# Kernel optimization log

Measured on AMD Instinct MI355X. Metric: run time of the kernel, lower is better.

## Reference

```python
import jax, jax.numpy as jnp
import numpy as np

EPS = 1e-6

def wave_repr(x, global_mode):
    # x: [B,S,D]
    x = jnp.clip(x, -10.0, 10.0)
    xsq = x * x
    if global_mode:
        Gsq = jnp.sum(xsq, axis=(1, 2), keepdims=True) + EPS  # [B,1,1]
    else:
        Gsq = jnp.sum(xsq, axis=1, keepdims=True) + EPS       # [B,1,D]
    G = jnp.maximum(jnp.sqrt(Gsq), EPS)
    # NOTE: source uses torch.div(..., rounding_mode='floor') -> floor division
    ratio = jnp.clip(jnp.floor(x / G), -0.99, 0.99)
    sqrt_term = jnp.sqrt(jnp.maximum(1.0 - ratio * ratio, EPS))
    alpha = jnp.arctan2(sqrt_term, ratio)
    return G * jnp.cos(alpha), G * jnp.sin(alpha)

def gelu(x):
    return jax.nn.gelu(x, approximate=False)

def rmsnorm(x, w):
    return x * jax.lax.rsqrt(jnp.mean(x * x, axis=-1, keepdims=True) + EPS) * w

def setup_inputs() -> dict:
    key = jax.random.key(0)
    B, S, D = 4, 4096, 1024
    ks = jax.random.split(key, 16)
    s = 0.02
    p = {
        'x': jax.random.normal(ks[0], (B, S, D), jnp.float32),
        'Wa': jax.random.normal(ks[1], (D, D)) * s, 'ba': jnp.zeros((D,)),
        'Wp': jax.random.normal(ks[2], (D, D)) * s, 'bp': jnp.zeros((D,)),
        'gate_bias': jnp.zeros((D,)),
        'w1r': jax.random.normal(ks[3], (D, 4 * D)) * s, 'b1r': jnp.zeros((4 * D,)),
        'w2r': jax.random.normal(ks[4], (4 * D, D)) * s, 'b2r': jnp.zeros((D,)),
        'w1i': jax.random.normal(ks[5], (D, 4 * D)) * s, 'b1i': jnp.zeros((4 * D,)),
        'w2i': jax.random.normal(ks[6], (4 * D, D)) * s, 'b2i': jnp.zeros((D,)),
        'We': jax.random.normal(ks[7], (2 * D, D)) * s, 'be': jnp.zeros((D,)),
        'g_rms': jnp.ones((D,)),
        'wf1': jax.random.normal(ks[8], (D, 2 * D)) * s, 'bf1': jnp.zeros((2 * D,)),
        'wf2': jax.random.normal(ks[9], (2 * D, D)) * s, 'bf2': jnp.zeros((D,)),
    }
    return p

def reference(x, Wa, ba, Wp, bp, gate_bias, w1r, b1r, w2r, b2r, w1i, b1i, w2i, b2i, We, be, g_rms, wf1, bf1, wf2, bf2):
    # wave representations: global (sentence) + local (token)
    rs, is_ = wave_repr(x, True)
    rt, it = wave_repr(x, False)
    cr = rs + rt
    ci = is_ + it
    # amplitude / phase
    amp = jnp.sqrt(cr * cr + ci * ci + EPS)
    ph = jnp.arctan2(ci, cr)
    # biological noise gate (eval mode: no noise)
    gate = jax.nn.sigmoid(amp @ Wa + ba + ph @ Wp + bp + gate_bias)
    gr = cr * gate
    gi = ci * gate
    rp = gelu(gr @ w1r + b1r) @ w2r + b2r
    ip = gelu(gi @ w1i + b1i) @ w2i + b2i
    # combine to embedding + RMSNorm
    wave = jnp.concatenate([rp, ip], axis=-1) @ We + be
    out = rmsnorm(wave, g_rms)
    y = gelu(out @ wf1 + bf1) @ wf2 + bf2
    return y
```

## Files before the change

kernel.cpp:

```cpp
#include <hip/hip_runtime.h>
#include <cmath>

typedef _Float16 f16;
typedef _Float16 f16x8 __attribute__((ext_vector_type(8)));
typedef _Float16 f16x4 __attribute__((ext_vector_type(4)));
typedef float f32x4 __attribute__((ext_vector_type(4)));

#define EPSF 1e-6f

__device__ __forceinline__ void gload16(const f16* g, const f16* l) {
  __builtin_amdgcn_global_load_lds(
      (__attribute__((address_space(1))) void*)g,
      (__attribute__((address_space(3))) void*)l, 16, 0, 0);
}

__device__ __forceinline__ float fast_gelu(float u) {
  const float z = u * 0.70710678118654752f;
  const float az = fabsf(z);
  const float t = __builtin_amdgcn_rcpf(fmaf(0.3275911f, az, 1.0f));
  float p = 1.061405429f;
  p = fmaf(p, t, -1.453152027f);
  p = fmaf(p, t, 1.421413741f);
  p = fmaf(p, t, -0.284496736f);
  p = fmaf(p, t, 0.254829592f);
  p = p * t;
  const float e = __expf(-az * az);
  float er = fmaf(-p, e, 1.0f);
  er = copysignf(er, z);
  return 0.5f * u * (1.0f + er);
}

__global__ void wtr_k(const float* __restrict__ W, f16* __restrict__ WT, int K, int N) {
  __shared__ float t[32][33];
  const int nb = blockIdx.x * 32, kb = blockIdx.y * 32;
  const int tx = threadIdx.x, ty = threadIdx.y;
#pragma unroll
  for (int i = ty; i < 32; i += 8) t[i][tx] = W[(size_t)(kb + i) * N + nb + tx];
  __syncthreads();
#pragma unroll
  for (int i = ty; i < 32; i += 8) WT[(size_t)(nb + i) * K + kb + tx] = (f16)t[tx][i];
}

__global__ void cast_k(const float* __restrict__ W, f16* __restrict__ H) {
  const size_t i = (size_t)blockIdx.x * 256 + threadIdx.x;
  const float4 v = ((const float4*)W)[i];
  f16x4 o;
  o[0] = (f16)v.x; o[1] = (f16)v.y; o[2] = (f16)v.z; o[3] = (f16)v.w;
  ((f16x4*)H)[i] = o;
}

__global__ void colsq_k(const float* __restrict__ x, float* __restrict__ part) {
  const int d = blockIdx.x * 256 + threadIdx.x;
  const int sb = blockIdx.y;
  const int b = blockIdx.z;
  const float* p = x + ((size_t)b * 4096 + (size_t)sb * 256) * 1024 + d;
  float acc = 0.f;
#pragma unroll 4
  for (int s = 0; s < 256; ++s) {
    float v = p[(size_t)s * 1024];
    v = fminf(fmaxf(v, -10.f), 10.f);
    acc = fmaf(v, v, acc);
  }
  part[((size_t)b * 16 + sb) * 1024 + d] = acc;
}

__global__ void stats_k(const float* __restrict__ part, float* __restrict__ Gsum,
                        float* __restrict__ amp) {
  const int b = blockIdx.x;
  const int t = threadIdx.x;
  __shared__ double red[256];
  float cs[4];
  double tot = 0.0;
#pragma unroll
  for (int i = 0; i < 4; ++i) {
    const int d = t + i * 256;
    double s = 0.0;
    for (int k = 0; k < 16; ++k) s += (double)part[((size_t)b * 16 + k) * 1024 + d];
    cs[i] = (float)s;
    tot += s;
  }
  red[t] = tot;
  __syncthreads();
  for (int st = 128; st > 0; st >>= 1) {
    if (t < st) red[t] += red[t + st];
    __syncthreads();
  }
  const float Gs = fmaxf(sqrtf((float)red[0] + EPSF), EPSF);
#pragma unroll
  for (int i = 0; i < 4; ++i) {
    const int d = t + i * 256;
    const float Gt = fmaxf(sqrtf(cs[i] + EPSF), EPSF);
    const float gs = Gs + Gt;
    Gsum[(b << 10) + d] = gs;
    amp[(b << 10) + d] = sqrtf(gs * gs + EPSF);
  }
}

__global__ void rtp_k(const float* __restrict__ amp, const float* __restrict__ Wa,
                      double* __restrict__ part) {
  const int d = blockIdx.x * 256 + threadIdx.x;
  const int b = blockIdx.y;
  const int kc = blockIdx.z;
  const float* a = amp + (b << 10);
  double acc = 0.0;
  for (int jj = 0; jj < 128; ++jj) {
    const int k = kc * 128 + jj;
    acc += (double)a[k] * (double)Wa[((size_t)k << 10) + d];
  }
  part[(((size_t)b * 8 + kc) << 10) + d] = acc;
}
__global__ void rtr_k(const double* __restrict__ part, const float* __restrict__ ba,
                      const float* __restrict__ bp, const float* __restrict__ gbias,
                      float* __restrict__ rt) {
  const int d = blockIdx.x * 256 + threadIdx.x;
  const int b = blockIdx.y;
  double acc = 0.0;
#pragma unroll
  for (int kc = 0; kc < 8; ++kc) acc += part[(((size_t)b * 8 + kc) << 10) + d];
  rt[(b << 10) + d] = (float)acc + ba[d] + bp[d] + gbias[d];
}

__global__ void bcp_k(const float* __restrict__ b2r, const float* __restrict__ b2i,
                      const float* __restrict__ We, double* __restrict__ part) {
  const int n = blockIdx.x * 256 + threadIdx.x;
  const int kc = blockIdx.y;
  double acc = 0.0;
  for (int jj = 0; jj < 128; ++jj) {
    const int j = kc * 128 + jj;
    const float bv = (j < 1024) ? b2r[j] : b2i[j - 1024];
    acc += (double)bv * (double)We[(size_t)j * 1024 + n];
  }
  part[((size_t)kc << 10) + n] = acc;
}
__global__ void bcr_k(const double* __restrict__ part, const float* __restrict__ be,
                      float* __restrict__ bc) {
  const int n = blockIdx.x * 256 + threadIdx.x;
  double acc = 0.0;
#pragma unroll
  for (int kc = 0; kc < 16; ++kc) acc += part[((size_t)kc << 10) + n];
  bc[n] = (float)acc + be[n];
}

__global__ void ph_k(const float* __restrict__ x, f16* __restrict__ ph, float phPos,
                     float phNeg) {
  const size_t i = (size_t)blockIdx.x * 256 + threadIdx.x;
  const float4 v = ((const float4*)x)[i];
  f16x4 o;
  o[0] = (f16)(v.x < 0.f ? phNeg : phPos);
  o[1] = (f16)(v.y < 0.f ? phNeg : phPos);
  o[2] = (f16)(v.z < 0.f ? phNeg : phPos);
  o[3] = (f16)(v.w < 0.f ? phNeg : phPos);
  ((f16x4*)ph)[i] = o;
}

__global__ void rms_k(const float* __restrict__ wave, const float* __restrict__ g,
                      f16* __restrict__ o) {
  const size_t row = blockIdx.x;
  const int t = threadIdx.x;
  const float4 v = ((const float4*)(wave + row * 1024))[t];
  float ss = v.x * v.x + v.y * v.y + v.z * v.z + v.w * v.w;
#pragma unroll
  for (int s = 32; s > 0; s >>= 1) ss += __shfl_down(ss, s);
  __shared__ float red[4];
  if ((t & 63) == 0) red[t >> 6] = ss;
  __syncthreads();
  const float tot = red[0] + red[1] + red[2] + red[3];
  const float r = rsqrtf(tot * (1.f / 1024.f) + EPSF);
  const float4 gv = ((const float4*)g)[t];
  f16x4 ov;
  ov[0] = (f16)(v.x * r * gv.x);
  ov[1] = (f16)(v.y * r * gv.y);
  ov[2] = (f16)(v.z * r * gv.z);
  ov[3] = (f16)(v.w * r * gv.w);
  ((f16x4*)(o + row * 1024))[t] = ov;
}

template <int EPI>
__global__ __launch_bounds__(512, 4) void gemm2_k(
    const f16* __restrict__ A, int lda, const f16* __restrict__ BT, int ldb, int K,
    const float* __restrict__ bias, float* __restrict__ outF, f16* __restrict__ outH,
    int ldo, const f16* __restrict__ phm, const float* __restrict__ rowterm,
    const float* __restrict__ Gsum, f16* __restrict__ gr, f16* __restrict__ gi, int r0,
    float ratioNeg, float stNeg) {
  __shared__ __align__(16) char smem[49152];
  f16(*smA)[4096] = reinterpret_cast<f16(*)[4096]>(smem);
  f16(*smB)[8192] = reinterpret_cast<f16(*)[8192]>(smem + 16384);
  const int tid = threadIdx.x;
  const int w = tid >> 6, l = tid & 63;

  const int ncol = gridDim.y;
  const int bid = blockIdx.x * ncol + blockIdx.y;
  const int nwg = gridDim.x * ncol;
  const int q = nwg >> 3, rr = nwg & 7;
  const int xcd = bid & 7, idx = bid >> 3;
  const int swz = (xcd < rr ? xcd * (q + 1) : rr * (q + 1) + (xcd - rr) * q) + idx;
  const int bx = swz / ncol, by = swz % ncol;
  const size_t rbase = (size_t)bx * 128;
  const size_t cbase = (size_t)by * 256;

  const int srow = (w << 4) + (l >> 2);
  const int slot = l & 3;
  const int ss = ((slot ^ ((srow >> 1) & 3)) << 3);

  f32x4 acc[4][4];
  const f32x4 zero = {0.f, 0.f, 0.f, 0.f};
#pragma unroll
  for (int m = 0; m < 4; ++m)
#pragma unroll
    for (int n = 0; n < 4; ++n) acc[m][n] = zero;

  const f16* gA = A + (rbase + srow) * (size_t)lda + ss;
  const f16* gB0 = BT + (cbase + srow) * (size_t)ldb + ss;
  const f16* gB1 = BT + (cbase + srow + 128) * (size_t)ldb + ss;

  const int nk = K >> 5;
  auto stage = [&](int buf, size_t ko) {
    gload16(gA + ko, &smA[buf][w << 9]);
    gload16(gB0 + ko, &smB[buf][w << 9]);
    gload16(gB1 + ko, &smB[buf][4096 + (w << 9)]);
  };
  stage(0, 0);
  __syncthreads();

  const int arow = l & 15;
  const int kg = (((l >> 4) ^ ((arow >> 1) & 3)) << 3);
  const int wr = (w >> 2) << 6;
  const int wc = (w & 3) << 6;

  for (int t = 0; t < nk; ++t) {
    const int cur = t & 1;
    if (t + 1 < nk) stage(cur ^ 1, (size_t)(t + 1) << 5);
    const f16* ap = &smA[cur][(wr + arow) * 32 + kg];
    const f16* bp = &smB[cur][(wc + arow) * 32 + kg];
    f16x8 af[4], bf[4];
#pragma unroll
    for (int m = 0; m < 4; ++m) af[m] = *(const f16x8*)(ap + m * 512);
#pragma unroll
    for (int n = 0; n < 4; ++n) bf[n] = *(const f16x8*)(bp + n * 512);
#pragma unroll
    for (int m = 0; m < 4; ++m)
#pragma unroll
      for (int n = 0; n < 4; ++n)
        acc[m][n] = __builtin_amdgcn_mfma_f32_16x16x32_f16(af[m], bf[n], acc[m][n], 0, 0, 0);
    __syncthreads();
  }

  const int fr = l & 15, hi = l >> 4;
  const int r4 = hi << 2;

  if constexpr (EPI == 3 || EPI == 5) {
    float* ep = reinterpret_cast<float*>(smem + w * 4352);
#pragma unroll
    for (int m = 0; m < 4; ++m) {
#pragma unroll
      for (int n = 0; n < 4; ++n) {
        const int cl = n * 16 + fr;
#pragma unroll
        for (int j = 0; j < 4; ++j) {
          float v = acc[m][n][j];
          if constexpr (EPI == 3) v = fast_gelu(v + bias[cbase + wc + cl]);
          ep[(r4 + j) * 65 + cl] = v;
        }
      }
      asm volatile("s_waitcnt lgkmcnt(0)" ::: "memory");
      __builtin_amdgcn_sched_barrier(0);
#pragma unroll
      for (int it = 0; it < 2; ++it) {
        const int rl = l >> 2;
        const int ch = (l & 3) + it * 4;
        const float* pr = &ep[rl * 65 + ch * 8];
        f16x8 o;
#pragma unroll
        for (int e = 0; e < 8; ++e) o[e] = (f16)pr[e];
        *(f16x8*)&outH[(rbase + wr + m * 16 + rl) * (size_t)ldo + (cbase + wc + ch * 8)] = o;
      }
      asm volatile("s_waitcnt lgkmcnt(0)" ::: "memory");
      __builtin_amdgcn_sched_barrier(0);
    }
  } else if constexpr (EPI == 4) {
    float* ep = reinterpret_cast<float*>(smem + w * 4352);
#pragma unroll
    for (int m = 0; m < 4; ++m) {
      float grv[4][4], giv[4][4];
#pragma unroll
      for (int n = 0; n < 4; ++n) {
        const size_t col = cbase + wc + n * 16 + fr;
#pragma unroll
        for (int j = 0; j < 4; ++j) {
          const size_t row = rbase + wr + m * 16 + r4 + j;
          const int gb = (int)(((size_t)r0 + row) >> 12);
          const float pre = acc[m][n][j] + rowterm[((size_t)gb << 10) + col];
          const float gate = __builtin_amdgcn_rcpf(1.f + __expf(-pre));
          const float ph = (float)phm[row * 1024 + col];
          const bool neg = ph > 2.f;
          const float gs = Gsum[((size_t)gb << 10) + col];
          grv[n][j] = (neg ? gs * ratioNeg : 0.f) * gate;
          giv[n][j] = gs * (neg ? stNeg : 1.f) * gate;
        }
      }
#pragma unroll
      for (int pass = 0; pass < 2; ++pass) {
        f16* dst = pass ? gi : gr;
#pragma unroll
        for (int n = 0; n < 4; ++n)
#pragma unroll
          for (int j = 0; j < 4; ++j)
            ep[(r4 + j) * 65 + n * 16 + fr] = pass ? giv[n][j] : grv[n][j];
        asm volatile("s_waitcnt lgkmcnt(0)" ::: "memory");
        __builtin_amdgcn_sched_barrier(0);
#pragma unroll
        for (int it = 0; it < 2; ++it) {
          const int rl = l >> 2;
          const int ch = (l & 3) + it * 4;
          const float* pr = &ep[rl * 65 + ch * 8];
          f16x8 o;
#pragma unroll
          for (int e = 0; e < 8; ++e) o[e] = (f16)pr[e];
          *(f16x8*)&dst[(rbase + wr + m * 16 + rl) * 1024 + (cbase + wc + ch * 8)] = o;
        }
        asm volatile("s_waitcnt lgkmcnt(0)" ::: "memory");
        __builtin_amdgcn_sched_barrier(0);
      }
    }
  } else {
#pragma unroll
    for (int m = 0; m < 4; ++m) {
#pragma unroll
      for (int n = 0; n < 4; ++n) {
        const size_t col = cbase + wc + n * 16 + fr;
#pragma unroll
        for (int j = 0; j < 4; ++j) {
          const size_t row = rbase + wr + m * 16 + r4 + j;
          const float v = acc[m][n][j];
          if constexpr (EPI == 0) {
            outF[row * (size_t)ldo + col] = v + bias[col];
          } else {
            outF[row * (size_t)ldo + col] += v;
          }
        }
      }
    }
  }
}

extern "C" void kernel_launch(void* const* d_in, const int* in_sizes, int n_in,
                              void* d_out, int out_size, void* d_ws, size_t ws_size,
                              hipStream_t stream) {
  const float* x     = (const float*)d_in[0];
  const float* Wa    = (const float*)d_in[1];
  const float* ba    = (const float*)d_in[2];
  const float* Wp    = (const float*)d_in[3];
  const float* bp    = (const float*)d_in[4];
  const float* gbias = (const float*)d_in[5];
  const float* w1r   = (const float*)d_in[6];
  const float* b1r   = (const float*)d_in[7];
  const float* w2r   = (const float*)d_in[8];
  const float* b2r   = (const float*)d_in[9];
  const float* w1i   = (const float*)d_in[10];
  const float* b1i   = (const float*)d_in[11];
  const float* w2i   = (const float*)d_in[12];
  const float* b2i   = (const float*)d_in[13];
  const float* We    = (const float*)d_in[14];
  const float* be    = (const float*)d_in[15];
  const float* grms  = (const float*)d_in[16];
  const float* wf1   = (const float*)d_in[17];
  const float* bf1   = (const float*)d_in[18];
  const float* wf2   = (const float*)d_in[19];
  const float* bf2   = (const float*)d_in[20];
  float* out = (float*)d_out;

  char* ws = (char*)d_ws;
  size_t off = 0;
  auto alloc = [&](size_t bytes) -> void* {
    void* p = (void*)(ws + off);
    off += (bytes + 255) & ~(size_t)255;
    return p;
  };

  f16* WpT   = (f16*)alloc((size_t)1024 * 1024 * 2);
  f16* w1rT  = (f16*)alloc((size_t)4096 * 1024 * 2);
  f16* w1iT  = (f16*)alloc((size_t)4096 * 1024 * 2);
  f16* wf1T  = (f16*)alloc((size_t)2048 * 1024 * 2);
  f16* wf2T  = (f16*)alloc((size_t)1024 * 2048 * 2);
  f16* WcrT  = (f16*)alloc((size_t)1024 * 4096 * 2);
  f16* WciT  = (f16*)alloc((size_t)1024 * 4096 * 2);
  float* part    = (float*)alloc((size_t)4 * 16 * 1024 * 4);
  float* GsumB   = (float*)alloc((size_t)4 * 1024 * 4);
  float* ampB    = (float*)alloc((size_t)4 * 1024 * 4);
  float* rowterm = (float*)alloc((size_t)4 * 1024 * 4);
  float* bcB     = (float*)alloc((size_t)1024 * 4);
  double* rtPart = (double*)alloc((size_t)4 * 8 * 1024 * 8);
  double* bcPart = (double*)alloc((size_t)16 * 1024 * 8);
  const size_t staticEnd = off;

  char* tmp = ws + staticEnd;
  f16* WeT  = (f16*)tmp;
  f16* w2rH = (f16*)(tmp + (size_t)4 * 1024 * 1024);
  f16* w2iH = (f16*)(tmp + (size_t)12 * 1024 * 1024);

  {
    dim3 b(32, 8);
    wtr_k<<<dim3(32, 32), b, 0, stream>>>(Wp, WpT, 1024, 1024);
    wtr_k<<<dim3(128, 32), b, 0, stream>>>(w1r, w1rT, 1024, 4096);
    wtr_k<<<dim3(128, 32), b, 0, stream>>>(w1i, w1iT, 1024, 4096);
    wtr_k<<<dim3(64, 32), b, 0, stream>>>(wf1, wf1T, 1024, 2048);
    wtr_k<<<dim3(32, 64), b, 0, stream>>>(wf2, wf2T, 2048, 1024);
    wtr_k<<<dim3(32, 64), b, 0, stream>>>(We, WeT, 2048, 1024);
    cast_k<<<dim3(4096), 256, 0, stream>>>(w2r, w2rH);
    cast_k<<<dim3(4096), 256, 0, stream>>>(w2i, w2iH);
  }

  colsq_k<<<dim3(4, 16, 4), 256, 0, stream>>>(x, part);
  stats_k<<<4, 256, 0, stream>>>(part, GsumB, ampB);
  rtp_k<<<dim3(4, 4, 8), 256, 0, stream>>>(ampB, Wa, rtPart);
  rtr_k<<<dim3(4, 4), 256, 0, stream>>>(rtPart, ba, bp, gbias, rowterm);
  bcp_k<<<dim3(4, 16), 256, 0, stream>>>(b2r, b2i, We, bcPart);
  bcr_k<<<dim3(4), 256, 0, stream>>>(bcPart, be, bcB);

  gemm2_k<5><<<dim3(8, 16), 512, 0, stream>>>(WeT, 2048, w2rH, 1024, 1024, nullptr,
      nullptr, WcrT, 4096, nullptr, nullptr, nullptr, nullptr, nullptr, 0, 0.f, 0.f);
  gemm2_k<5><<<dim3(8, 16), 512, 0, stream>>>(WeT + 1024, 2048, w2iH, 1024, 1024, nullptr,
      nullptr, WciT, 4096, nullptr, nullptr, nullptr, nullptr, nullptr, 0, 0.f, 0.f);

  const float ratioNeg = -0.99f;
  const float stNeg = sqrtf(fmaxf(1.0f - 0.99f * 0.99f, EPSF));
  const float phPos = atan2f(1.0f, 0.0f);
  const float phNeg = atan2f(stNeg, ratioNeg);

  const long Ntok = (long)in_sizes[0] / 1024;
  const size_t perRow = 14336;
  long R = (long)((ws_size > staticEnd ? ws_size - staticEnd : 0) / perRow);
  R &= ~255L;
  if (R > Ntok) R = Ntok;
  if (R < 256) R = 256;

  char* cb = ws + staticEnd;
  f16* phB = (f16*)cb;
  f16* grB = (f16*)(cb + (size_t)R * 2048);
  f16* giB = (f16*)(cb + (size_t)R * 4096);
  f16* h1B = (f16*)(cb + (size_t)R * 6144);
  float* waveF = (float*)phB;
  f16* outB = giB;
  f16* h2B = h1B;

  for (long r0 = 0; r0 < Ntok; r0 += R) {
    const long Rc = (Ntok - r0 < R) ? (Ntok - r0) : R;
    const int gm = (int)(Rc / 128);
    ph_k<<<dim3((int)Rc), 256, 0, stream>>>(x + r0 * 1024, phB, phPos, phNeg);
    gemm2_k<4><<<dim3(gm, 4), 512, 0, stream>>>(phB, 1024, WpT, 1024, 1024, nullptr,
        nullptr, nullptr, 1024, phB, rowterm, GsumB, grB, giB, (int)r0, ratioNeg, stNeg);
    gemm2_k<3><<<dim3(gm, 16), 512, 0, stream>>>(grB, 1024, w1rT, 1024, 1024, b1r,
        nullptr, h1B, 4096, nullptr, nullptr, nullptr, nullptr, nullptr, 0, 0.f, 0.f);
    gemm2_k<0><<<dim3(gm, 4), 512, 0, stream>>>(h1B, 4096, WcrT, 4096, 4096, bcB,
        waveF, nullptr, 1024, nullptr, nullptr, nullptr, nullptr, nullptr, 0, 0.f, 0.f);
    gemm2_k<3><<<dim3(gm, 16), 512, 0, stream>>>(giB, 1024, w1iT, 1024, 1024, b1i,
        nullptr, h1B, 4096, nullptr, nullptr, nullptr, nullptr, nullptr, 0, 0.f, 0.f);
    gemm2_k<1><<<dim3(gm, 4), 512, 0, stream>>>(h1B, 4096, WciT, 4096, 4096, nullptr,
        waveF, nullptr, 1024, nullptr, nullptr, nullptr, nullptr, nullptr, 0, 0.f, 0.f);
    rms_k<<<dim3((int)Rc), 256, 0, stream>>>(waveF, grms, outB);
    gemm2_k<3><<<dim3(gm, 8), 512, 0, stream>>>(outB, 1024, wf1T, 1024, 1024, bf1,
        nullptr, h2B, 2048, nullptr, nullptr, nullptr, nullptr, nullptr, 0, 0.f, 0.f);
    gemm2_k<0><<<dim3(gm, 4), 512, 0, stream>>>(h2B, 2048, wf2T, 2048, 2048, bf2,
        out + r0 * 1024, nullptr, 1024, nullptr, nullptr, nullptr, nullptr, nullptr, 0, 0.f, 0.f);
  }
}
```

Before: 1.312 ms.

## Add 256x256-tile 4-stage pipelined GEMM for GELU up-projection layers

Adds a new GEMM kernel with 256x256 output tiles, a 4-deep LDS ring buffer filled by direct global-to-LDS loads, XCD-aware block swizzling, and an LDS-staged epilogue that writes f16 rows with 16-byte vector stores. It replaces the 128-row GEMM for the three up-projections that apply GELU. The larger tiles raise arithmetic intensity and the deeper prefetch hides load latency. The cost is 128KB of dynamic shared memory and a grid of half as many row blocks, which may lower occupancy, and the chunk row count must now be a multiple of 256.

```diff
diff --git a/kernel.cpp b/kernel.cpp
--- a/kernel.cpp
+++ b/kernel.cpp
@@ -340,6 +340,129 @@
         }
       }
     }
+  }
+}
+
+template <int EPI>
+__global__ __launch_bounds__(512, 2) void gemm4_k(
+    const f16* __restrict__ A, int lda, const f16* __restrict__ BT, int ldb, int K,
+    const float* __restrict__ bias, f16* __restrict__ outH, int ldo) {
+  extern __shared__ __align__(16) char smem4[];
+  f16* sm = (f16*)smem4;
+  const int tid = threadIdx.x;
+  const int w = tid >> 6, l = tid & 63;
+
+  const int ncol = gridDim.y;
+  const int bid = blockIdx.x * ncol + blockIdx.y;
+  const int nwg = gridDim.x * ncol;
+  const int q = nwg >> 3, rr = nwg & 7;
+  const int xcd = bid & 7, idx = bid >> 3;
+  const int swz = (xcd < rr ? xcd * (q + 1) : rr * (q + 1) + (xcd - rr) * q) + idx;
+  const int bx = swz / ncol, by = swz % ncol;
+  const size_t rbase = (size_t)bx * 256;
+  const size_t cbase = (size_t)by * 256;
+
+  const int srow = w * 16 + (l >> 2);
+  const int gsl = (((l & 3) ^ ((l >> 2) & 3)) << 3);
+  const f16* gA = A + (rbase + srow) * (size_t)lda + gsl;
+  const f16* gB = BT + (cbase + srow) * (size_t)ldb + gsl;
+
+  auto stageA = [&](int buf, int t) {
+    const size_t kb = (size_t)t << 5;
+    f16* d = sm + buf * 16384 + (w * 16) * 32;
+    gload16(gA + kb, d);
+    gload16(gA + kb + (size_t)128 * lda, d + 4096);
+  };
+  auto stageB = [&](int buf, int t) {
+    const size_t kb = (size_t)t << 5;
+    f16* d = sm + buf * 16384 + 8192 + (w * 16) * 32;
+    gload16(gB + kb, d);
+    gload16(gB + kb + (size_t)128 * ldb, d + 4096);
+  };
+
+  f32x4 acc[8][4];
+  const f32x4 zero = {0.f, 0.f, 0.f, 0.f};
+#pragma unroll
+  for (int m = 0; m < 8; ++m)
+#pragma unroll
+    for (int n = 0; n < 4; ++n) acc[m][n] = zero;
+
+  const int nt = K >> 5;
+  stageA(0, 0); stageB(0, 0);
+  stageA(1, 1); stageB(1, 1);
+  stageA(2, 2); stageB(2, 2);
+  asm volatile("s_waitcnt vmcnt(8)" ::: "memory");
+  __builtin_amdgcn_s_barrier();
+
+  const int fr = l & 15, hi = l >> 4;
+  const int px = ((hi ^ (fr & 3)) << 3);
+  const int wm = w >> 2, wn = w & 3;
+
+  for (int t = 0; t < nt; ++t) {
+    const int bb = (t & 3) * 16384;
+    const int sb = (t + 3) & 3;
+    const int st = (t + 3 < nt) ? (t + 3) : (nt - 1);
+    const f16* pa = sm + bb + (wm * 128 + fr) * 32 + px;
+    const f16* pb = sm + bb + 8192 + (wn * 64 + fr) * 32 + px;
+    f16x8 af[4], bf[4];
+#pragma unroll
+    for (int m = 0; m < 4; ++m) af[m] = *(const f16x8*)(pa + m * 512);
+#pragma unroll
+    for (int n = 0; n < 4; ++n) bf[n] = *(const f16x8*)(pb + n * 512);
+    stageA(sb, st);
+    __builtin_amdgcn_s_setprio(1);
+#pragma unroll
+    for (int m = 0; m < 4; ++m)
+#pragma unroll
+      for (int n = 0; n < 4; ++n)
+        acc[m][n] = __builtin_amdgcn_mfma_f32_16x16x32_f16(af[m], bf[n], acc[m][n], 0, 0, 0);
+    __builtin_amdgcn_s_setprio(0);
+#pragma unroll
+    for (int m = 0; m < 4; ++m) af[m] = *(const f16x8*)(pa + 2048 + m * 512);
+    stageB(sb, st);
+    __builtin_amdgcn_s_setprio(1);
+#pragma unroll
+    for (int m = 0; m < 4; ++m)
+#pragma unroll
+      for (int n = 0; n < 4; ++n)
+        acc[4 + m][n] = __builtin_amdgcn_mfma_f32_16x16x32_f16(af[m], bf[n], acc[4 + m][n], 0, 0, 0);
+    __builtin_amdgcn_s_setprio(0);
+    asm volatile("s_waitcnt vmcnt(8)" ::: "memory");
+    __builtin_amdgcn_s_barrier();
+  }
+
+  asm volatile("s_waitcnt vmcnt(0)" ::: "memory");
+  __builtin_amdgcn_s_barrier();
+
+  const int r4 = hi << 2;
+  float* ep = (float*)(smem4 + w * 4352);
+#pragma unroll
+  for (int am = 0; am < 8; ++am) {
+#pragma unroll
+    for (int n = 0; n < 4; ++n) {
+      const int cl = n * 16 + fr;
+#pragma unroll
+      for (int j = 0; j < 4; ++j) {
+        float v = acc[am][n][j];
+        if constexpr (EPI == 3) v = fast_gelu(v + bias[cbase + wn * 64 + cl]);
+        ep[(r4 + j) * 65 + cl] = v;
+      }
+    }
+    asm volatile("s_waitcnt lgkmcnt(0)" ::: "memory");
+    __builtin_amdgcn_sched_barrier(0);
+#pragma unroll
+    for (int it = 0; it < 2; ++it) {
+      const int rl = l >> 2;
+      const int ch = (l & 3) + it * 4;
+      const float* pr = &ep[rl * 65 + ch * 8];
+      f16x8 o;
+#pragma unroll
+      for (int e = 0; e < 8; ++e) o[e] = (f16)pr[e];
+      *(f16x8*)&outH[(rbase + wm * 128 + am * 16 + rl) * (size_t)ldo +
+                     (cbase + wn * 64 + ch * 8)] = o;
+    }
+    asm volatile("s_waitcnt lgkmcnt(0)" ::: "memory");
+    __builtin_amdgcn_sched_barrier(0);
   }
 }
 
@@ -369,6 +492,9 @@
   const float* bf2   = (const float*)d_in[20];
   float* out = (float*)d_out;
 
+  hipFuncSetAttribute((const void*)gemm4_k<3>, hipFuncAttributeMaxDynamicSharedMemorySize,
+                      131072);
+
   char* ws = (char*)d_ws;
   size_t off = 0;
   auto alloc = [&](size_t bytes) -> void* {
@@ -446,20 +572,21 @@
   for (long r0 = 0; r0 < Ntok; r0 += R) {
     const long Rc = (Ntok - r0 < R) ? (Ntok - r0) : R;
     const int gm = (int)(Rc / 128);
+    const int gm4 = (int)(Rc / 256);
     ph_k<<<dim3((int)Rc), 256, 0, stream>>>(x + r0 * 1024, phB, phPos, phNeg);
     gemm2_k<4><<<dim3(gm, 4), 512, 0, stream>>>(phB, 1024, WpT, 1024, 1024, nullptr,
         nullptr, nullptr, 1024, phB, rowterm, GsumB, grB, giB, (int)r0, ratioNeg, stNeg);
-    gemm2_k<3><<<dim3(gm, 16), 512, 0, stream>>>(grB, 1024, w1rT, 1024, 1024, b1r,
-        nullptr, h1B, 4096, nullptr, nullptr, nullptr, nullptr, nullptr, 0, 0.f, 0.f);
+    gemm4_k<3><<<dim3(gm4, 16), 512, 131072, stream>>>(grB, 1024, w1rT, 1024, 1024, b1r,
+        h1B, 4096);
     gemm2_k<0><<<dim3(gm, 4), 512, 0, stream>>>(h1B, 4096, WcrT, 4096, 4096, bcB,
         waveF, nullptr, 1024, nullptr, nullptr, nullptr, nullptr, nullptr, 0, 0.f, 0.f);
-    gemm2_k<3><<<dim3(gm, 16), 512, 0, stream>>>(giB, 1024, w1iT, 1024, 1024, b1i,
-        nullptr, h1B, 4096, nullptr, nullptr, nullptr, nullptr, nullptr, 0, 0.f, 0.f);
+    gemm4_k<3><<<dim3(gm4, 16), 512, 131072, stream>>>(giB, 1024, w1iT, 1024, 1024, b1i,
+        h1B, 4096);
     gemm2_k<1><<<dim3(gm, 4), 512, 0, stream>>>(h1B, 4096, WciT, 4096, 4096, nullptr,
         waveF, nullptr, 1024, nullptr, nullptr, nullptr, nullptr, nullptr, 0, 0.f, 0.f);
     rms_k<<<dim3((int)Rc), 256, 0, stream>>>(waveF, grms, outB);
-    gemm2_k<3><<<dim3(gm, 8), 512, 0, stream>>>(outB, 1024, wf1T, 1024, 1024, bf1,
-        nullptr, h2B, 2048, nullptr, nullptr, nullptr, nullptr, nullptr, 0, 0.f, 0.f);
+    gemm4_k<3><<<dim3(gm4, 8), 512, 131072, stream>>>(outB, 1024, wf1T, 1024, 1024, bf1,
+        h2B, 2048);
     gemm2_k<0><<<dim3(gm, 4), 512, 0, stream>>>(h2B, 2048, wf2T, 2048, 2048, bf2,
         out + r0 * 1024, nullptr, 1024, nullptr, nullptr, nullptr, nullptr, nullptr, 0, 0.f, 0.f);
   }
```

After: 1.333 ms. No clear change (+1.6%).
